# Kernel tuning notes

Hardware: AMD Instinct MI355X
Metric: run time of the kernel (lower is better)

Reference implementation:

```python
import jax, jax.numpy as jnp
import numpy as np

V, E, H, Z = 32000, 256, 512, 64
B, T = 32, 128
PAD = 0


def _n(k, shape, s=0.05):
    return jax.random.normal(k, shape, jnp.float32) * s


def setup_inputs() -> dict:
    key = jax.random.key(0)
    ks = jax.random.split(key, 32)
    inp = {
        "x": jax.random.randint(ks[0], (B, T), 0, V),
        "y": jax.random.randint(ks[1], (B, T), 0, V),
        "epsilon": jax.random.normal(ks[2], (Z,), jnp.float32),
        "enc_emb": _n(ks[3], (V, E)).at[PAD].set(0.0),  # padding_idx row zeroed
        "dec_emb": _n(ks[4], (V, E)),
        "fwd_Wih": _n(ks[5], (4 * H, E)), "fwd_Whh": _n(ks[6], (4 * H, H)), "fwd_b": _n(ks[7], (4 * H,)),
        "bwd_Wih": _n(ks[8], (4 * H, E)), "bwd_Whh": _n(ks[9], (4 * H, H)), "bwd_b": _n(ks[10], (4 * H,)),
        "dec_Wih": _n(ks[11], (4 * H, E)), "dec_Whh": _n(ks[12], (4 * H, H)), "dec_b": _n(ks[13], (4 * H,)),
        "enc_hW": _n(ks[14], (H, 2 * H)), "enc_hb": _n(ks[15], (H,)),
        "mu_W": _n(ks[16], (Z, H)), "mu_b": _n(ks[17], (Z,)),
        "std_W": _n(ks[18], (Z, H)), "std_b": _n(ks[19], (Z,)),
        "dec_hW": _n(ks[20], (H, Z)), "dec_hb": _n(ks[21], (H,)),
        "out_W": _n(ks[22], (V, H)), "out_b": _n(ks[23], (V,)),
    }
    return inp


def lstm_scan(e, h0, c0, Wih, Whh, b):
    # e: [B,T,E]; returns all hidden states [B,T,H] and final (h,c)
    def step(carry, x_t):
        h, c = carry
        g = x_t @ Wih.T + h @ Whh.T + b  # [B,4H], torch gate order i,f,g,o
        i, f, gg, o = jnp.split(g, 4, axis=-1)
        c = jax.nn.sigmoid(f) * c + jax.nn.sigmoid(i) * jnp.tanh(gg)
        h = jax.nn.sigmoid(o) * jnp.tanh(c)
        return (h, c), h
    (hT, cT), hs = jax.lax.scan(step, (h0, c0), jnp.swapaxes(e, 0, 1))
    return jnp.swapaxes(hs, 0, 1), hT, cT


def reference(x, y, epsilon, enc_emb, dec_emb,
              fwd_Wih, fwd_Whh, fwd_b, bwd_Wih, bwd_Whh, bwd_b,
              dec_Wih, dec_Whh, dec_b, enc_hW, enc_hb,
              mu_W, mu_b, std_W, std_b, dec_hW, dec_hb, out_W, out_b):
    Bx = x.shape[0]
    zeros = jnp.zeros((Bx, H), jnp.float32)
    # ---- encoder: two unidirectional LSTMs (second over flipped seq) ----
    ef = enc_emb[x]                 # [B,T,E]
    eb = enc_emb[x[:, ::-1]]
    _, hf, _ = lstm_scan(ef, zeros, zeros, fwd_Wih, fwd_Whh, fwd_b)
    _, hb, _ = lstm_scan(eb, zeros, zeros, bwd_Wih, bwd_Whh, bwd_b)
    h = jnp.concatenate([hf, hb], axis=1) @ enc_hW.T + enc_hb  # [B,H] (no activation)
    mu = h @ mu_W.T + mu_b
    sigma = jax.nn.softplus(h @ std_W.T + std_b)
    # ---- reparameterization (single epsilon shared across batch, as in torch) ----
    z = mu + sigma * epsilon        # [B,Z]
    # ---- decoder ----
    h0 = jnp.tanh(z @ dec_hW.T + dec_hb)  # [B,H]
    ed = dec_emb[x]
    hs, _, _ = lstm_scan(ed, h0, jnp.zeros_like(h0), dec_Wih, dec_Whh, dec_b)  # [B,T,H]
    logits = hs @ out_W.T + out_b   # [B,T,V]
    # ---- losses ----
    logp = jax.nn.log_softmax(logits.reshape(-1, V), axis=-1)
    ce = -jnp.take_along_axis(logp, y.reshape(-1, 1), axis=1).sum()
    kl = -0.5 * (1.0 + jnp.log(sigma) - mu ** 2 - sigma).sum()
    return (kl + ce) / Bx
```

## Files before the change

kernel.cpp:

```cpp
#include <hip/hip_runtime.h>
#include <hip/hip_bf16.h>

typedef float f32x4 __attribute__((ext_vector_type(4)));
typedef short s16x8 __attribute__((ext_vector_type(8)));
typedef unsigned int u32;
typedef unsigned short u16;

#define DEV static __device__ __forceinline__

namespace {
constexpr int V = 32000, E = 256, H = 512, Z = 64, B = 32, T = 128;
constexpr u32 POISON = 0xFFFFFFFFu;
constexpr int GUARD = 1 << 20;

constexpr size_t OFF_ZF   = 0;
constexpr size_t OFF_ZB   = 32768;
constexpr size_t OFF_PF   = 65536;
constexpr size_t OFF_PB   = OFF_PF + (size_t)T * 32768;
constexpr size_t OFF_H0   = OFF_PB + (size_t)T * 32768;
constexpr size_t OFF_HENC = OFF_H0 + 32768;
constexpr size_t OFF_HS   = OFF_HENC + 32768;
constexpr size_t OFF_LGY  = OFF_HS + (size_t)B*T*H*2;
constexpr size_t OFF_CER  = OFF_LGY + 16384;
constexpr size_t OFF_PEND = OFF_CER + 16384;
constexpr size_t OFF_Z    = OFF_PEND;
constexpr size_t OFF_KLP  = OFF_Z + 8192;
constexpr size_t OFF_WB   = OFF_KLP + 256;
constexpr size_t OFF_CEP  = OFF_PF;
}

DEV u16 f2b(float f) {
  u32 x = __builtin_bit_cast(u32, f);
  return (u16)((x + 0x7fffu + ((x >> 16) & 1u)) >> 16);
}
DEV float b2f(u16 u) {
  u32 x = ((u32)u) << 16;
  return __builtin_bit_cast(float, x);
}
DEV float fsig(float x) { return 1.f / (1.f + __expf(-x)); }
DEV float ftanh(float x) { return 2.f / (1.f + __expf(-2.f * x)) - 1.f; }

DEV u32 aload(const u32* p) { return __hip_atomic_load(p, __ATOMIC_RELAXED, __HIP_MEMORY_SCOPE_AGENT); }
DEV void astore(u32* p, u32 v) { __hip_atomic_store(p, v, __ATOMIC_RELAXED, __HIP_MEMORY_SCOPE_AGENT); }
DEV void afstore(u32* p, float v) { astore(p, __builtin_bit_cast(u32, v)); }

DEV u32* hslot(char* ws, int dir, int s) {
  size_t off = (s == 0) ? (dir ? OFF_ZB : OFF_ZF)
                        : ((dir ? OFF_PB : OFF_PF) + (size_t)(s - 1) * 32768);
  return reinterpret_cast<u32*>(ws + off);
}

__global__ __launch_bounds__(512, 1) void phaseA_k(
    const int* __restrict__ x, const float* __restrict__ emb,
    const float* __restrict__ fWih, const float* __restrict__ fWhh, const float* __restrict__ fb,
    const float* __restrict__ bWih, const float* __restrict__ bWhh, const float* __restrict__ bb,
    const float* __restrict__ enc_hW, const float* __restrict__ enc_hb,
    const float* __restrict__ mu_W, const float* __restrict__ mu_b,
    const float* __restrict__ std_W, const float* __restrict__ std_b,
    const float* __restrict__ epsv, const float* __restrict__ out_W,
    char* __restrict__ ws)
{
  __shared__ __align__(16) u16 Wl[64][776];
  __shared__ __align__(16) u16 act[32][776];
  __shared__ __align__(16) float gates[64][33];

  const int tid = threadIdx.x;
  const int wg = blockIdx.x;

  if (wg >= 64) {
    const size_t total = (size_t)V * H / 8;
    for (size_t idx = (size_t)(wg - 64) * 512 + tid; idx < total; idx += (size_t)128 * 512) {
      const float4* src = reinterpret_cast<const float4*>(out_W + idx * 8);
      float4 a = src[0], b = src[1];
      s16x8 o;
      o[0] = (short)f2b(a.x); o[1] = (short)f2b(a.y); o[2] = (short)f2b(a.z); o[3] = (short)f2b(a.w);
      o[4] = (short)f2b(b.x); o[5] = (short)f2b(b.y); o[6] = (short)f2b(b.z); o[7] = (short)f2b(b.w);
      *reinterpret_cast<s16x8*>(ws + OFF_WB + idx * 16) = o;
    }
    return;
  }

  const bool bwd = wg >= 32;
  const int dir = bwd ? 1 : 0;
  const int lw = wg & 31;
  const int u0 = lw * 16;
  const float* Wih = bwd ? bWih : fWih;
  const float* Whh = bwd ? bWhh : fWhh;
  const float* bv  = bwd ? bb : fb;

  {
    int r = tid >> 3, s8 = tid & 7;
    int grow = (r & 3) * H + u0 + (r >> 2);
    for (int kc = s8 * 96; kc < s8 * 96 + 96; kc += 8) {
      const float4* p;
      if (kc < E) p = reinterpret_cast<const float4*>(Wih + (size_t)grow * E + kc);
      else        p = reinterpret_cast<const float4*>(Whh + (size_t)grow * H + (kc - E));
      float4 a = p[0], b4 = p[1];
      Wl[r][kc+0] = f2b(a.x);  Wl[r][kc+1] = f2b(a.y);  Wl[r][kc+2] = f2b(a.z);  Wl[r][kc+3] = f2b(a.w);
      Wl[r][kc+4] = f2b(b4.x); Wl[r][kc+5] = f2b(b4.y); Wl[r][kc+6] = f2b(b4.z); Wl[r][kc+7] = f2b(b4.w);
    }
  }

  const int ab = tid >> 4, au = tid & 15;
  const int wv = tid >> 6, lane = tid & 63, l15 = lane & 15, lhi = lane >> 4;
  const int mq = wv & 3, nh = wv >> 2;
  const int unit = u0 + mq * 4 + lhi;
  const int batch = nh * 16 + l15;
  const float Bi = bv[0*H + unit], Bf = bv[1*H + unit];
  const float Bg = bv[2*H + unit], Bo = bv[3*H + unit];
  float c = 0.f;
  u32* actu = reinterpret_cast<u32*>(&act[0][0]);

  auto stage_emb = [&](int t) {
    int tt = bwd ? (T - 1 - t) : t;
    const float* src = emb + (size_t)x[ab * T + tt] * E + au * 16;
    const float4* s4 = reinterpret_cast<const float4*>(src);
    float4 A0 = s4[0], A1 = s4[1], A2 = s4[2], A3 = s4[3];
    u32 w0 = f2b(A0.x) | ((u32)f2b(A0.y) << 16);
    u32 w1 = f2b(A0.z) | ((u32)f2b(A0.w) << 16);
    u32 w2 = f2b(A1.x) | ((u32)f2b(A1.y) << 16);
    u32 w3 = f2b(A1.z) | ((u32)f2b(A1.w) << 16);
    u32 w4 = f2b(A2.x) | ((u32)f2b(A2.y) << 16);
    u32 w5 = f2b(A2.z) | ((u32)f2b(A2.w) << 16);
    u32 w6 = f2b(A3.x) | ((u32)f2b(A3.y) << 16);
    u32 w7 = f2b(A3.z) | ((u32)f2b(A3.w) << 16);
    u32* dst = actu + ab * 388 + au * 8;
    reinterpret_cast<uint4*>(dst)[0] = make_uint4(w0, w1, w2, w3);
    reinterpret_cast<uint4*>(dst)[1] = make_uint4(w4, w5, w6, w7);
  };

  stage_emb(0);

  for (int t = 0; t < T; ++t) {
    {
      const u32* hsrc = hslot(ws, dir, t);
      u32 tmp[16];
      #pragma unroll
      for (int j = 0; j < 16; ++j) tmp[j] = aload(hsrc + tid + j * 512);
      int guard = 0;
      while (true) {
        bool bad = false;
        #pragma unroll
        for (int j = 0; j < 16; ++j)
          if (tmp[j] == POISON) { bad = true; tmp[j] = aload(hsrc + tid + j * 512); }
        if (!bad || ++guard > GUARD) break;
        __builtin_amdgcn_s_sleep(1);
      }
      #pragma unroll
      for (int j = 0; j < 16; ++j) {
        int i = tid + j * 512;
        actu[(i >> 8) * 388 + 128 + (i & 255)] = tmp[j];
      }
    }
    __syncthreads();

    {
      f32x4 ac0 = {0,0,0,0}, ac1 = {0,0,0,0}, ac2 = {0,0,0,0}, ac3 = {0,0,0,0};
      #pragma unroll
      for (int s = 0; s < 6; ++s) {
        int kk = s * 128 + lhi * 8;
        s16x8 A0 = *reinterpret_cast<const s16x8*>(&Wl[mq * 16 + l15][kk]);
        s16x8 B0 = *reinterpret_cast<const s16x8*>(&act[nh * 16 + l15][kk]);
        ac0 = __builtin_amdgcn_mfma_f32_16x16x32_bf16(A0, B0, ac0, 0, 0, 0);
        s16x8 A1 = *reinterpret_cast<const s16x8*>(&Wl[mq * 16 + l15][kk + 32]);
        s16x8 B1 = *reinterpret_cast<const s16x8*>(&act[nh * 16 + l15][kk + 32]);
        ac1 = __builtin_amdgcn_mfma_f32_16x16x32_bf16(A1, B1, ac1, 0, 0, 0);
        s16x8 A2 = *reinterpret_cast<const s16x8*>(&Wl[mq * 16 + l15][kk + 64]);
        s16x8 B2 = *reinterpret_cast<const s16x8*>(&act[nh * 16 + l15][kk + 64]);
        ac2 = __builtin_amdgcn_mfma_f32_16x16x32_bf16(A2, B2, ac2, 0, 0, 0);
        s16x8 A3 = *reinterpret_cast<const s16x8*>(&Wl[mq * 16 + l15][kk + 96]);
        s16x8 B3 = *reinterpret_cast<const s16x8*>(&act[nh * 16 + l15][kk + 96]);
        ac3 = __builtin_amdgcn_mfma_f32_16x16x32_bf16(A3, B3, ac3, 0, 0, 0);
      }
      f32x4 ac = (ac0 + ac1) + (ac2 + ac3);
      float gi = ac[0] + Bi, gf = ac[1] + Bf, gg = ac[2] + Bg, go = ac[3] + Bo;
      c = fsig(gf) * c + fsig(gi) * ftanh(gg);
      float h = fsig(go) * ftanh(c);
      u32 bits = f2b(h);
      u32 other = (u32)__shfl_down((int)bits, 16);
      if ((lhi & 1) == 0) {
        u32* dst = hslot(ws, dir, t + 1) + batch * 256 + (unit >> 1);
        astore(dst, bits | (other << 16));
      }
    }
    __syncthreads();
    if (t != T - 1) stage_emb(t + 1);
  }

  {
    u32* wlu = reinterpret_cast<u32*>(&Wl[0][0]);
    const u32* hf = hslot(ws, 0, T);
    const u32* hb = hslot(ws, 1, T);
    u32 tmp[32];
    #pragma unroll
    for (int j = 0; j < 32; ++j) {
      int i = tid + j * 512, b = i >> 9, k = i & 511;
      tmp[j] = (k < 256) ? aload(hf + b * 256 + k) : aload(hb + b * 256 + (k - 256));
    }
    int guard = 0;
    while (true) {
      bool bad = false;
      #pragma unroll
      for (int j = 0; j < 32; ++j)
        if (tmp[j] == POISON) {
          bad = true;
          int i = tid + j * 512, b = i >> 9, k = i & 511;
          tmp[j] = (k < 256) ? aload(hf + b * 256 + k) : aload(hb + b * 256 + (k - 256));
        }
      if (!bad || ++guard > GUARD) break;
      __builtin_amdgcn_s_sleep(1);
    }
    #pragma unroll
    for (int j = 0; j < 32; ++j) wlu[tid + j * 512] = tmp[j];
  }
  __syncthreads();
  if (tid < 256) {
    const u16* hcat = &Wl[0][0];
    int b = tid >> 3, jc = tid & 7;
    int j = wg * 8 + jc;
    float s = enc_hb[j];
    const float4* w4 = reinterpret_cast<const float4*>(enc_hW + (size_t)j * 1024);
    for (int kk = 0; kk < 256; ++kk) {
      float4 wv4 = w4[kk];
      const u16* hp = hcat + b * 1024 + kk * 4;
      s += wv4.x * b2f(hp[0]) + wv4.y * b2f(hp[1]) + wv4.z * b2f(hp[2]) + wv4.w * b2f(hp[3]);
    }
    u32 bits = f2b(s);
    u32 other = (u32)__shfl_down((int)bits, 1);
    if ((jc & 1) == 0) {
      u32* dst = reinterpret_cast<u32*>(ws + OFF_HENC) + b * 256 + j / 2;
      astore(dst, bits | (other << 16));
    }
  }
  __syncthreads();

  {
    u32* hhu = reinterpret_cast<u32*>(&act[0][0]);
    const u32* he = reinterpret_cast<const u32*>(ws + OFF_HENC);
    u32 tmp[16];
    #pragma unroll
    for (int j = 0; j < 16; ++j) tmp[j] = aload(he + tid + j * 512);
    int guard = 0;
    while (true) {
      bool bad = false;
      #pragma unroll
      for (int j = 0; j < 16; ++j)
        if (tmp[j] == POISON) { bad = true; tmp[j] = aload(he + tid + j * 512); }
      if (!bad || ++guard > GUARD) break;
      __builtin_amdgcn_s_sleep(1);
    }
    #pragma unroll
    for (int j = 0; j < 16; ++j) hhu[tid + j * 512] = tmp[j];
  }
  __syncthreads();
  {
    const u16* hh = &act[0][0];
    int b = tid >> 4, l16 = tid & 15;
    float pm = 0.f, ps = 0.f;
    const float* mwr = mu_W + (size_t)wg * H;
    const float* swr = std_W + (size_t)wg * H;
    for (int k = l16 * 32; k < l16 * 32 + 32; ++k) {
      float hv = b2f(hh[b * H + k]);
      pm += mwr[k] * hv;
      ps += swr[k] * hv;
    }
    gates[b][l16] = pm;
    gates[32 + b][l16] = ps;
  }
  __syncthreads();
  if (tid < 32) {
    int b = tid;
    float mu = mu_b[wg], sv = std_b[wg];
    for (int l = 0; l < 16; ++l) { mu += gates[b][l]; sv += gates[32 + b][l]; }
    float sig = fmaxf(sv, 0.f) + log1pf(__expf(-fabsf(sv)));
    float zv = mu + sig * epsv[wg];
    reinterpret_cast<float*>(ws + OFF_Z)[b * Z + wg] = zv;
    gates[b][16] = -0.5f * (1.f + logf(sig) - mu * mu - sig);
  }
  __syncthreads();
  if (tid == 0) {
    float kl = 0.f;
    for (int b = 0; b < 32; ++b) kl += gates[b][16];
    reinterpret_cast<float*>(ws + OFF_KLP)[wg] = kl;
  }
}

__global__ __launch_bounds__(512, 1) void phaseB_k(
    const int* __restrict__ x, const int* __restrict__ y,
    const float* __restrict__ emb,
    const float* __restrict__ Wih, const float* __restrict__ Whh, const float* __restrict__ bv,
    const float* __restrict__ dec_hW, const float* __restrict__ dec_hb,
    const float* __restrict__ out_W, const float* __restrict__ out_b,
    char* __restrict__ ws, float* __restrict__ out)
{
  __shared__ __align__(16) char smem[157440];
  const int tid = threadIdx.x;
  const int bid = blockIdx.x;
  u32* hsu = reinterpret_cast<u32*>(ws + OFF_HS);
  const int wid = tid >> 6, lane = tid & 63, l15 = lane & 15, lhi = lane >> 4;

  if (bid < 32) {
    u16 (*Wl)[776]  = reinterpret_cast<u16(*)[776]>(smem);
    u16 (*act)[776] = reinterpret_cast<u16(*)[776]>(smem + 99328);
    const int wg = bid;
    const int u0 = wg * 16;

    {
      int r = tid >> 3, s8 = tid & 7;
      int grow = (r & 3) * H + u0 + (r >> 2);
      for (int kc = s8 * 96; kc < s8 * 96 + 96; kc += 8) {
        const float4* p;
        if (kc < E) p = reinterpret_cast<const float4*>(Wih + (size_t)grow * E + kc);
        else        p = reinterpret_cast<const float4*>(Whh + (size_t)grow * H + (kc - E));
        float4 a = p[0], b4 = p[1];
        Wl[r][kc+0] = f2b(a.x);  Wl[r][kc+1] = f2b(a.y);  Wl[r][kc+2] = f2b(a.z);  Wl[r][kc+3] = f2b(a.w);
        Wl[r][kc+4] = f2b(b4.x); Wl[r][kc+5] = f2b(b4.y); Wl[r][kc+6] = f2b(b4.z); Wl[r][kc+7] = f2b(b4.w);
      }
    }

    const int ab = tid >> 4, au = tid & 15;
    const int mq = wid & 3, nh = wid >> 2;
    const int unit = u0 + mq * 4 + lhi;
    const int batch = nh * 16 + l15;
    const float Bi = bv[0*H + unit], Bf = bv[1*H + unit];
    const float Bg = bv[2*H + unit], Bo = bv[3*H + unit];
    float c = 0.f;

    u32* h0u = reinterpret_cast<u32*>(ws + OFF_H0);
    const float* zws = reinterpret_cast<const float*>(ws + OFF_Z);
    u32* actu = reinterpret_cast<u32*>(&act[0][0]);

    auto stage_emb = [&](int t) {
      const float* src = emb + (size_t)x[ab * T + t] * E + au * 16;
      const float4* s4 = reinterpret_cast<const float4*>(src);
      float4 A0 = s4[0], A1 = s4[1], A2 = s4[2], A3 = s4[3];
      u32 w0 = f2b(A0.x) | ((u32)f2b(A0.y) << 16);
      u32 w1 = f2b(A0.z) | ((u32)f2b(A0.w) << 16);
      u32 w2 = f2b(A1.x) | ((u32)f2b(A1.y) << 16);
      u32 w3 = f2b(A1.z) | ((u32)f2b(A1.w) << 16);
      u32 w4 = f2b(A2.x) | ((u32)f2b(A2.y) << 16);
      u32 w5 = f2b(A2.z) | ((u32)f2b(A2.w) << 16);
      u32 w6 = f2b(A3.x) | ((u32)f2b(A3.y) << 16);
      u32 w7 = f2b(A3.z) | ((u32)f2b(A3.w) << 16);
      u32* dst = actu + ab * 388 + au * 8;
      reinterpret_cast<uint4*>(dst)[0] = make_uint4(w0, w1, w2, w3);
      reinterpret_cast<uint4*>(dst)[1] = make_uint4(w4, w5, w6, w7);
    };

    stage_emb(0);

    {
      float s = dec_hb[u0 + au];
      const float* wr = dec_hW + (size_t)(u0 + au) * Z;
      for (int zz = 0; zz < Z; ++zz) s += wr[zz] * zws[ab * Z + zz];
      float h0 = ftanh(s);
      u32 bits = f2b(h0);
      u32 other = (u32)__shfl_down((int)bits, 1);
      if ((au & 1) == 0) astore(h0u + ab * 256 + (u0 + au) / 2, bits | (other << 16));
    }

    for (int t = 0; t < T; ++t) {
      {
        u32 tmp[16];
        const u32* base = (t == 0) ? h0u : (hsu + (size_t)(t - 1) * B * 256);
        #pragma unroll
        for (int j = 0; j < 16; ++j) tmp[j] = aload(base + tid + j * 512);
        int guard = 0;
        while (true) {
          bool bad = false;
          #pragma unroll
          for (int j = 0; j < 16; ++j)
            if (tmp[j] == POISON) { bad = true; tmp[j] = aload(base + tid + j * 512); }
          if (!bad || ++guard > GUARD) break;
          __builtin_amdgcn_s_sleep(1);
        }
        #pragma unroll
        for (int j = 0; j < 16; ++j) {
          int i = tid + j * 512;
          actu[(i >> 8) * 388 + 128 + (i & 255)] = tmp[j];
        }
      }
      __syncthreads();

      {
        f32x4 ac0 = {0,0,0,0}, ac1 = {0,0,0,0}, ac2 = {0,0,0,0}, ac3 = {0,0,0,0};
        #pragma unroll
        for (int s = 0; s < 6; ++s) {
          int kk = s * 128 + lhi * 8;
          s16x8 A0 = *reinterpret_cast<const s16x8*>(&Wl[mq * 16 + l15][kk]);
          s16x8 B0 = *reinterpret_cast<const s16x8*>(&act[nh * 16 + l15][kk]);
          ac0 = __builtin_amdgcn_mfma_f32_16x16x32_bf16(A0, B0, ac0, 0, 0, 0);
          s16x8 A1 = *reinterpret_cast<const s16x8*>(&Wl[mq * 16 + l15][kk + 32]);
          s16x8 B1 = *reinterpret_cast<const s16x8*>(&act[nh * 16 + l15][kk + 32]);
          ac1 = __builtin_amdgcn_mfma_f32_16x16x32_bf16(A1, B1, ac1, 0, 0, 0);
          s16x8 A2 = *reinterpret_cast<const s16x8*>(&Wl[mq * 16 + l15][kk + 64]);
          s16x8 B2 = *reinterpret_cast<const s16x8*>(&act[nh * 16 + l15][kk + 64]);
          ac2 = __builtin_amdgcn_mfma_f32_16x16x32_bf16(A2, B2, ac2, 0, 0, 0);
          s16x8 A3 = *reinterpret_cast<const s16x8*>(&Wl[mq * 16 + l15][kk + 96]);
          s16x8 B3 = *reinterpret_cast<const s16x8*>(&act[nh * 16 + l15][kk + 96]);
          ac3 = __builtin_amdgcn_mfma_f32_16x16x32_bf16(A3, B3, ac3, 0, 0, 0);
        }
        f32x4 ac = (ac0 + ac1) + (ac2 + ac3);
        float gi = ac[0] + Bi, gf = ac[1] + Bf, gg = ac[2] + Bg, go = ac[3] + Bo;
        c = fsig(gf) * c + fsig(gi) * ftanh(gg);
        float h = fsig(go) * ftanh(c);
        u32 bits = f2b(h);
        u32 other = (u32)__shfl_down((int)bits, 16);
        if ((lhi & 1) == 0) {
          u32* dst = hsu + (size_t)(t * B + batch) * 256 + (unit >> 1);
          astore(dst, bits | (other << 16));
        }
      }
      __syncthreads();
      if (t != T - 1) stage_emb(t + 1);
    }
    return;
  }

  const int w = bid - 32;
  u16 (*At)[72] = reinterpret_cast<u16(*)[72]>(smem);
  u16 (*Bt)[72] = reinterpret_cast<u16(*)[72]>(smem + 18432);
  float* red = reinterpret_cast<float*>(smem + 55296);
  const u16* Wb = reinterpret_cast<const u16*>(ws + OFF_WB);
  const int wm = wid & 1, wn = wid >> 1;
  const int sr = tid >> 3, ss = tid & 7;

  for (int tl = w; tl < 4000; tl += 192) {
    const int rt = tl / 125, ct = tl % 125;
    const int row0 = rt * 128, col0 = ct * 256;

    f32x4 acc[4][4];
    #pragma unroll
    for (int i = 0; i < 4; ++i)
      #pragma unroll
      for (int j = 0; j < 4; ++j) acc[i][j] = {0, 0, 0, 0};

    for (int kt = 0; kt < 8; ++kt) {
      #pragma unroll
      for (int it = 0; it < 2; ++it) {
        int r = it * 64 + sr;
        const u32* p = hsu + (size_t)(row0 + r) * 256 + kt * 32 + ss * 4;
        u32 a0 = aload(p), a1 = aload(p + 1), a2 = aload(p + 2), a3 = aload(p + 3);
        int guard = 0;
        while ((a0 == POISON || a1 == POISON || a2 == POISON || a3 == POISON) && ++guard <= GUARD) {
          __builtin_amdgcn_s_sleep(64);
          a0 = aload(p); a1 = aload(p + 1); a2 = aload(p + 2); a3 = aload(p + 3);
        }
        u32* d = reinterpret_cast<u32*>(&At[r][ss * 8]);
        d[0] = a0; d[1] = a1; d[2] = a2; d[3] = a3;
      }
      #pragma unroll
      for (int it = 0; it < 4; ++it) {
        int r = it * 64 + sr;
        *reinterpret_cast<s16x8*>(&Bt[r][ss * 8]) =
            *reinterpret_cast<const s16x8*>(Wb + (size_t)(col0 + r) * H + kt * 64 + ss * 8);
      }
      __syncthreads();
      #pragma unroll
      for (int ks = 0; ks < 2; ++ks) {
        int kk = ks * 32 + lhi * 8;
        s16x8 af[4], bf[4];
        #pragma unroll
        for (int mi = 0; mi < 4; ++mi)
          af[mi] = *reinterpret_cast<const s16x8*>(&At[wm * 64 + mi * 16 + l15][kk]);
        #pragma unroll
        for (int ni = 0; ni < 4; ++ni)
          bf[ni] = *reinterpret_cast<const s16x8*>(&Bt[wn * 64 + ni * 16 + l15][kk]);
        #pragma unroll
        for (int mi = 0; mi < 4; ++mi)
          #pragma unroll
          for (int ni = 0; ni < 4; ++ni)
            acc[mi][ni] = __builtin_amdgcn_mfma_f32_16x16x32_bf16(af[mi], bf[ni], acc[mi][ni], 0, 0, 0);
      }
      __syncthreads();
    }

    float bias[4];
    #pragma unroll
    for (int ni = 0; ni < 4; ++ni) bias[ni] = out_b[col0 + wn * 64 + ni * 16 + l15];

    #pragma unroll
    for (int mi = 0; mi < 4; ++mi) {
      #pragma unroll
      for (int reg = 0; reg < 4; ++reg) {
        float l0 = acc[mi][0][reg] + bias[0];
        float l1 = acc[mi][1][reg] + bias[1];
        float l2 = acc[mi][2][reg] + bias[2];
        float l3 = acc[mi][3][reg] + bias[3];
        float m = fmaxf(fmaxf(l0, l1), fmaxf(l2, l3));
        for (int d = 1; d < 16; d <<= 1) m = fmaxf(m, __shfl_xor(m, d, 16));
        float s = __expf(l0 - m) + __expf(l1 - m) + __expf(l2 - m) + __expf(l3 - m);
        for (int d = 1; d < 16; d <<= 1) s += __shfl_xor(s, d, 16);
        if (l15 == 0) {
          int lr = mi * 16 + lhi * 4 + reg;
          red[((wm * 64 + lr) * 4 + wn) * 2 + 0] = m;
          red[((wm * 64 + lr) * 4 + wn) * 2 + 1] = s;
        }
      }
    }
    __syncthreads();
    if (tid < 128) {
      int lr = tid;
      float M = -3.0e38f, S = 0.f;
      #pragma unroll
      for (int wnn = 0; wnn < 4; ++wnn) {
        float m = red[(lr * 4 + wnn) * 2 + 0];
        float s = red[(lr * 4 + wnn) * 2 + 1];
        float nm = fmaxf(M, m);
        S = S * __expf(M - nm) + s * __expf(m - nm);
        M = nm;
      }
      u32* cepw = reinterpret_cast<u32*>(ws + OFF_CEP);
      size_t ix = ((size_t)(row0 + lr) * 125 + ct) * 2;
      afstore(cepw + ix + 0, M);
      afstore(cepw + ix + 1, S);
    }
    __syncthreads();
  }

  for (int r = w * 8 + wid; r < 4096; r += 192 * 8) {
    int t = r >> 5, b = r & 31;
    int yy = y[b * T + t];
    const u32* hp = hsu + (size_t)r * 256 + lane * 4;
    u32 a0 = aload(hp), a1 = aload(hp + 1), a2 = aload(hp + 2), a3 = aload(hp + 3);
    int guard = 0;
    while ((a0 == POISON || a1 == POISON || a2 == POISON || a3 == POISON) && ++guard <= GUARD) {
      __builtin_amdgcn_s_sleep(64);
      a0 = aload(hp); a1 = aload(hp + 1); a2 = aload(hp + 2); a3 = aload(hp + 3);
    }
    const float4* wp = reinterpret_cast<const float4*>(out_W + (size_t)yy * H + lane * 8);
    float4 w0 = wp[0], w1 = wp[1];
    float s = b2f((u16)(a0 & 0xFFFF)) * w0.x + b2f((u16)(a0 >> 16)) * w0.y
            + b2f((u16)(a1 & 0xFFFF)) * w0.z + b2f((u16)(a1 >> 16)) * w0.w
            + b2f((u16)(a2 & 0xFFFF)) * w1.x + b2f((u16)(a2 >> 16)) * w1.y
            + b2f((u16)(a3 & 0xFFFF)) * w1.z + b2f((u16)(a3 >> 16)) * w1.w;
    for (int d = 1; d < 64; d <<= 1) s += __shfl_xor(s, d);
    if (lane == 0)
      afstore(reinterpret_cast<u32*>(ws + OFF_LGY) + r, s + out_b[yy]);
  }

  {
    int r = w * 512 + tid;
    if (r < 4096) {
      const u32* lgyu = reinterpret_cast<const u32*>(ws + OFF_LGY);
      u32 lb = aload(lgyu + r);
      int guard = 0;
      while (lb == POISON && ++guard <= GUARD) { __builtin_amdgcn_s_sleep(64); lb = aload(lgyu + r); }
      float ly = __builtin_bit_cast(float, lb);
      const u32* cp = reinterpret_cast<const u32*>(ws + OFF_CEP);
      float M = -3.0e38f, S = 0.f;
      for (int cch = 0; cch < 125; ++cch) {
        size_t ix = ((size_t)r * 125 + cch) * 2;
        u32 ma = aload(cp + ix), sa = aload(cp + ix + 1);
        int g2 = 0;
        while ((ma == POISON || sa == POISON) && ++g2 <= GUARD) {
          __builtin_amdgcn_s_sleep(64);
          ma = aload(cp + ix); sa = aload(cp + ix + 1);
        }
        float m = __builtin_bit_cast(float, ma), s = __builtin_bit_cast(float, sa);
        float nm = fmaxf(M, m);
        S = S * __expf(M - nm) + s * __expf(m - nm);
        M = nm;
      }
      afstore(reinterpret_cast<u32*>(ws + OFF_CER) + r, M + logf(S) - ly);
    }
  }

  if (w == 0) {
    __syncthreads();
    float* rb = reinterpret_cast<float*>(smem);
    const u32* ceru = reinterpret_cast<const u32*>(ws + OFF_CER);
    const float* klp = reinterpret_cast<const float*>(ws + OFF_KLP);
    float s = 0.f;
    for (int j = 0; j < 8; ++j) {
      int r = tid + j * 512;
      u32 v = aload(ceru + r);
      int guard = 0;
      while (v == POISON && ++guard <= GUARD) { __builtin_amdgcn_s_sleep(64); v = aload(ceru + r); }
      s += __builtin_bit_cast(float, v);
    }
    if (tid < 64) s += klp[tid];
    rb[tid] = s;
    __syncthreads();
    for (int d = 256; d > 0; d >>= 1) {
      if (tid < d) rb[tid] += rb[tid + d];
      __syncthreads();
    }
    if (tid == 0) out[0] = rb[0] / 32.f;
  }
}

extern "C" void kernel_launch(void* const* d_in, const int* in_sizes, int n_in,
                              void* d_out, int out_size, void* d_ws, size_t ws_size,
                              hipStream_t stream) {
  (void)in_sizes; (void)n_in; (void)out_size; (void)ws_size;
  const int*   x       = (const int*)d_in[0];
  const int*   y       = (const int*)d_in[1];
  const float* epsv    = (const float*)d_in[2];
  const float* enc_emb = (const float*)d_in[3];
  const float* dec_emb = (const float*)d_in[4];
  const float* fWih    = (const float*)d_in[5];
  const float* fWhh    = (const float*)d_in[6];
  const float* fb      = (const float*)d_in[7];
  const float* bWih    = (const float*)d_in[8];
  const float* bWhh    = (const float*)d_in[9];
  const float* bb      = (const float*)d_in[10];
  const float* dWih    = (const float*)d_in[11];
  const float* dWhh    = (const float*)d_in[12];
  const float* db      = (const float*)d_in[13];
  const float* enc_hW  = (const float*)d_in[14];
  const float* enc_hb  = (const float*)d_in[15];
  const float* mu_W    = (const float*)d_in[16];
  const float* mu_b    = (const float*)d_in[17];
  const float* std_W   = (const float*)d_in[18];
  const float* std_b   = (const float*)d_in[19];
  const float* dec_hW  = (const float*)d_in[20];
  const float* dec_hb  = (const float*)d_in[21];
  const float* out_W   = (const float*)d_in[22];
  const float* out_b   = (const float*)d_in[23];
  char* ws = (char*)d_ws;

  hipMemsetAsync(ws + OFF_ZF, 0x00, 65536, stream);
  hipMemsetAsync(ws + OFF_PF, 0xFF, OFF_PEND - OFF_PF, stream);

  phaseA_k<<<192, 512, 0, stream>>>(x, enc_emb, fWih, fWhh, fb, bWih, bWhh, bb,
                                    enc_hW, enc_hb, mu_W, mu_b, std_W, std_b,
                                    epsv, out_W, ws);

  hipMemsetAsync(ws + OFF_CEP, 0xFF, 4096000, stream);

  phaseB_k<<<224, 512, 0, stream>>>(x, y, dec_emb, dWih, dWhh, db, dec_hW, dec_hb,
                                    out_W, out_b, ws, (float*)d_out);
}
```

Measured before the change: 1.165 ms.

## Load recurrent hidden state directly into MFMA registers, transpose CE partial layout

In the encoder and decoder LSTM recurrences, each lane now polls and loads the exact previous hidden-state fragments it needs for its MFMA B operand straight from global memory into registers. This replaces cooperatively staging the whole h vector into shared memory and removes the barrier that staging required before the matmul. The shared activation buffer shrinks to hold only the embedding part. Separately, the cross-entropy partial (max, sum) array is stored column-chunk-major so the final reduction reads it coalesced across threads. In exchange, each lane issues more redundant global loads and holds 64 extra registers, and an extra barrier is added after staging the embedding.

```diff
diff --git a/kernel.cpp b/kernel.cpp
--- a/kernel.cpp
+++ b/kernel.cpp
@@ -5,6 +5,7 @@
 typedef short s16x8 __attribute__((ext_vector_type(8)));
 typedef unsigned int u32;
 typedef unsigned short u16;
+typedef u32 u32x4v __attribute__((ext_vector_type(4)));
 
 #define DEV static __device__ __forceinline__
 
@@ -50,6 +51,20 @@
   return reinterpret_cast<u32*>(ws + off);
 }
 
+DEV void pollload_h(const u32* hb_, int lhi, u32 (&hv)[64]) {
+  #pragma unroll
+  for (int i = 0; i < 64; ++i) hv[i] = aload(hb_ + (i >> 2) * 16 + lhi * 4 + (i & 3));
+  int guard = 0;
+  while (true) {
+    bool bad = false;
+    #pragma unroll
+    for (int i = 0; i < 64; ++i)
+      if (hv[i] == POISON) { bad = true; hv[i] = aload(hb_ + (i >> 2) * 16 + lhi * 4 + (i & 3)); }
+    if (!bad || ++guard > GUARD) break;
+    __builtin_amdgcn_s_sleep(1);
+  }
+}
+
 __global__ __launch_bounds__(512, 1) void phaseA_k(
     const int* __restrict__ x, const float* __restrict__ emb,
     const float* __restrict__ fWih, const float* __restrict__ fWhh, const float* __restrict__ fb,
@@ -61,7 +76,7 @@
     char* __restrict__ ws)
 {
   __shared__ __align__(16) u16 Wl[64][776];
-  __shared__ __align__(16) u16 act[32][776];
+  __shared__ __align__(16) u16 actE[32][256];
   __shared__ __align__(16) float gates[64][33];
 
   const int tid = threadIdx.x;
@@ -109,7 +124,7 @@
   const float Bi = bv[0*H + unit], Bf = bv[1*H + unit];
   const float Bg = bv[2*H + unit], Bo = bv[3*H + unit];
   float c = 0.f;
-  u32* actu = reinterpret_cast<u32*>(&act[0][0]);
+  u32* actu = reinterpret_cast<u32*>(&actE[0][0]);
 
   auto stage_emb = [&](int t) {
     int tt = bwd ? (T - 1 - t) : t;
@@ -124,56 +139,42 @@
     u32 w5 = f2b(A2.z) | ((u32)f2b(A2.w) << 16);
     u32 w6 = f2b(A3.x) | ((u32)f2b(A3.y) << 16);
     u32 w7 = f2b(A3.z) | ((u32)f2b(A3.w) << 16);
-    u32* dst = actu + ab * 388 + au * 8;
+    u32* dst = actu + ab * 128 + au * 8;
     reinterpret_cast<uint4*>(dst)[0] = make_uint4(w0, w1, w2, w3);
     reinterpret_cast<uint4*>(dst)[1] = make_uint4(w4, w5, w6, w7);
   };
 
   stage_emb(0);
+  __syncthreads();
+
+  const u16* wrow = &Wl[mq * 16 + l15][0];
+  const u16* arow = &actE[nh * 16 + l15][0];
 
   for (int t = 0; t < T; ++t) {
+    u32 hv[64];
+    pollload_h(hslot(ws, dir, t) + batch * 256, lhi, hv);
+
     {
-      const u32* hsrc = hslot(ws, dir, t);
-      u32 tmp[16];
-      #pragma unroll
-      for (int j = 0; j < 16; ++j) tmp[j] = aload(hsrc + tid + j * 512);
-      int guard = 0;
-      while (true) {
-        bool bad = false;
-        #pragma unroll
-        for (int j = 0; j < 16; ++j)
-          if (tmp[j] == POISON) { bad = true; tmp[j] = aload(hsrc + tid + j * 512); }
-        if (!bad || ++guard > GUARD) break;
-        __builtin_amdgcn_s_sleep(1);
-      }
-      #pragma unroll
-      for (int j = 0; j < 16; ++j) {
-        int i = tid + j * 512;
-        actu[(i >> 8) * 388 + 128 + (i & 255)] = tmp[j];
-      }
-    }
-    __syncthreads();
-
-    {
-      f32x4 ac0 = {0,0,0,0}, ac1 = {0,0,0,0}, ac2 = {0,0,0,0}, ac3 = {0,0,0,0};
-      #pragma unroll
-      for (int s = 0; s < 6; ++s) {
-        int kk = s * 128 + lhi * 8;
-        s16x8 A0 = *reinterpret_cast<const s16x8*>(&Wl[mq * 16 + l15][kk]);
-        s16x8 B0 = *reinterpret_cast<const s16x8*>(&act[nh * 16 + l15][kk]);
-        ac0 = __builtin_amdgcn_mfma_f32_16x16x32_bf16(A0, B0, ac0, 0, 0, 0);
-        s16x8 A1 = *reinterpret_cast<const s16x8*>(&Wl[mq * 16 + l15][kk + 32]);
-        s16x8 B1 = *reinterpret_cast<const s16x8*>(&act[nh * 16 + l15][kk + 32]);
-        ac1 = __builtin_amdgcn_mfma_f32_16x16x32_bf16(A1, B1, ac1, 0, 0, 0);
-        s16x8 A2 = *reinterpret_cast<const s16x8*>(&Wl[mq * 16 + l15][kk + 64]);
-        s16x8 B2 = *reinterpret_cast<const s16x8*>(&act[nh * 16 + l15][kk + 64]);
-        ac2 = __builtin_amdgcn_mfma_f32_16x16x32_bf16(A2, B2, ac2, 0, 0, 0);
-        s16x8 A3 = *reinterpret_cast<const s16x8*>(&Wl[mq * 16 + l15][kk + 96]);
-        s16x8 B3 = *reinterpret_cast<const s16x8*>(&act[nh * 16 + l15][kk + 96]);
-        ac3 = __builtin_amdgcn_mfma_f32_16x16x32_bf16(A3, B3, ac3, 0, 0, 0);
-      }
-      f32x4 ac = (ac0 + ac1) + (ac2 + ac3);
-      float gi = ac[0] + Bi, gf = ac[1] + Bf, gg = ac[2] + Bg, go = ac[3] + Bo;
+      f32x4 ac[4];
+      #pragma unroll
+      for (int i = 0; i < 4; ++i) ac[i] = {0, 0, 0, 0};
+      #pragma unroll
+      for (int fe = 0; fe < 8; ++fe) {
+        int kk = fe * 32 + lhi * 8;
+        s16x8 A = *reinterpret_cast<const s16x8*>(wrow + kk);
+        s16x8 Bv = *reinterpret_cast<const s16x8*>(arow + kk);
+        ac[fe & 3] = __builtin_amdgcn_mfma_f32_16x16x32_bf16(A, Bv, ac[fe & 3], 0, 0, 0);
+      }
+      #pragma unroll
+      for (int f = 0; f < 16; ++f) {
+        int kk = 256 + f * 32 + lhi * 8;
+        s16x8 A = *reinterpret_cast<const s16x8*>(wrow + kk);
+        u32x4v bw = {hv[4*f], hv[4*f+1], hv[4*f+2], hv[4*f+3]};
+        s16x8 Bv = __builtin_bit_cast(s16x8, bw);
+        ac[f & 3] = __builtin_amdgcn_mfma_f32_16x16x32_bf16(A, Bv, ac[f & 3], 0, 0, 0);
+      }
+      f32x4 acs = (ac[0] + ac[1]) + (ac[2] + ac[3]);
+      float gi = acs[0] + Bi, gf = acs[1] + Bf, gg = acs[2] + Bg, go = acs[3] + Bo;
       c = fsig(gf) * c + fsig(gi) * ftanh(gg);
       float h = fsig(go) * ftanh(c);
       u32 bits = f2b(h);
@@ -184,7 +185,7 @@
       }
     }
     __syncthreads();
-    if (t != T - 1) stage_emb(t + 1);
+    if (t != T - 1) { stage_emb(t + 1); __syncthreads(); }
   }
 
   {
@@ -235,7 +236,7 @@
   __syncthreads();
 
   {
-    u32* hhu = reinterpret_cast<u32*>(&act[0][0]);
+    u32* hhu = reinterpret_cast<u32*>(&Wl[0][0]);
     const u32* he = reinterpret_cast<const u32*>(ws + OFF_HENC);
     u32 tmp[16];
     #pragma unroll
@@ -249,12 +250,13 @@
       if (!bad || ++guard > GUARD) break;
       __builtin_amdgcn_s_sleep(1);
     }
+    __syncthreads();
     #pragma unroll
     for (int j = 0; j < 16; ++j) hhu[tid + j * 512] = tmp[j];
   }
   __syncthreads();
   {
-    const u16* hh = &act[0][0];
+    const u16* hh = &Wl[0][0];
     int b = tid >> 4, l16 = tid & 15;
     float pm = 0.f, ps = 0.f;
     const float* mwr = mu_W + (size_t)wg * H;
@@ -300,8 +302,8 @@
   const int wid = tid >> 6, lane = tid & 63, l15 = lane & 15, lhi = lane >> 4;
 
   if (bid < 32) {
-    u16 (*Wl)[776]  = reinterpret_cast<u16(*)[776]>(smem);
-    u16 (*act)[776] = reinterpret_cast<u16(*)[776]>(smem + 99328);
+    u16 (*Wl)[776]   = reinterpret_cast<u16(*)[776]>(smem);
+    u16 (*actE)[256] = reinterpret_cast<u16(*)[256]>(smem + 99328);
     const int wg = bid;
     const int u0 = wg * 16;
 
@@ -328,7 +330,7 @@
 
     u32* h0u = reinterpret_cast<u32*>(ws + OFF_H0);
     const float* zws = reinterpret_cast<const float*>(ws + OFF_Z);
-    u32* actu = reinterpret_cast<u32*>(&act[0][0]);
+    u32* actu = reinterpret_cast<u32*>(&actE[0][0]);
 
     auto stage_emb = [&](int t) {
       const float* src = emb + (size_t)x[ab * T + t] * E + au * 16;
@@ -342,7 +344,7 @@
       u32 w5 = f2b(A2.z) | ((u32)f2b(A2.w) << 16);
       u32 w6 = f2b(A3.x) | ((u32)f2b(A3.y) << 16);
       u32 w7 = f2b(A3.z) | ((u32)f2b(A3.w) << 16);
-      u32* dst = actu + ab * 388 + au * 8;
+      u32* dst = actu + ab * 128 + au * 8;
       reinterpret_cast<uint4*>(dst)[0] = make_uint4(w0, w1, w2, w3);
       reinterpret_cast<uint4*>(dst)[1] = make_uint4(w4, w5, w6, w7);
     };
@@ -358,50 +360,37 @@
       u32 other = (u32)__shfl_down((int)bits, 1);
       if ((au & 1) == 0) astore(h0u + ab * 256 + (u0 + au) / 2, bits | (other << 16));
     }
+    __syncthreads();
+
+    const u16* wrow = &Wl[mq * 16 + l15][0];
+    const u16* arow = &actE[nh * 16 + l15][0];
 
     for (int t = 0; t < T; ++t) {
+      const u32* base = (t == 0) ? h0u : (hsu + (size_t)(t - 1) * B * 256);
+      u32 hv[64];
+      pollload_h(base + batch * 256, lhi, hv);
+
       {
-        u32 tmp[16];
-        const u32* base = (t == 0) ? h0u : (hsu + (size_t)(t - 1) * B * 256);
+        f32x4 ac[4];
         #pragma unroll
-        for (int j = 0; j < 16; ++j) tmp[j] = aload(base + tid + j * 512);
-        int guard = 0;
-        while (true) {
-          bool bad = false;
-          #pragma unroll
-          for (int j = 0; j < 16; ++j)
-            if (tmp[j] == POISON) { bad = true; tmp[j] = aload(base + tid + j * 512); }
-          if (!bad || ++guard > GUARD) break;
-          __builtin_amdgcn_s_sleep(1);
+        for (int i = 0; i < 4; ++i) ac[i] = {0, 0, 0, 0};
+        #pragma unroll
+        for (int fe = 0; fe < 8; ++fe) {
+          int kk = fe * 32 + lhi * 8;
+          s16x8 A = *reinterpret_cast<const s16x8*>(wrow + kk);
+          s16x8 Bv = *reinterpret_cast<const s16x8*>(arow + kk);
+          ac[fe & 3] = __builtin_amdgcn_mfma_f32_16x16x32_bf16(A, Bv, ac[fe & 3], 0, 0, 0);
         }
         #pragma unroll
-        for (int j = 0; j < 16; ++j) {
-          int i = tid + j * 512;
-          actu[(i >> 8) * 388 + 128 + (i & 255)] = tmp[j];
+        for (int f = 0; f < 16; ++f) {
+          int kk = 256 + f * 32 + lhi * 8;
+          s16x8 A = *reinterpret_cast<const s16x8*>(wrow + kk);
+          u32x4v bw = {hv[4*f], hv[4*f+1], hv[4*f+2], hv[4*f+3]};
+          s16x8 Bv = __builtin_bit_cast(s16x8, bw);
+          ac[f & 3] = __builtin_amdgcn_mfma_f32_16x16x32_bf16(A, Bv, ac[f & 3], 0, 0, 0);
         }
-      }
-      __syncthreads();
-
-      {
-        f32x4 ac0 = {0,0,0,0}, ac1 = {0,0,0,0}, ac2 = {0,0,0,0}, ac3 = {0,0,0,0};
-        #pragma unroll
-        for (int s = 0; s < 6; ++s) {
-          int kk = s * 128 + lhi * 8;
-          s16x8 A0 = *reinterpret_cast<const s16x8*>(&Wl[mq * 16 + l15][kk]);
-          s16x8 B0 = *reinterpret_cast<const s16x8*>(&act[nh * 16 + l15][kk]);
-          ac0 = __builtin_amdgcn_mfma_f32_16x16x32_bf16(A0, B0, ac0, 0, 0, 0);
-          s16x8 A1 = *reinterpret_cast<const s16x8*>(&Wl[mq * 16 + l15][kk + 32]);
-          s16x8 B1 = *reinterpret_cast<const s16x8*>(&act[nh * 16 + l15][kk + 32]);
-          ac1 = __builtin_amdgcn_mfma_f32_16x16x32_bf16(A1, B1, ac1, 0, 0, 0);
-          s16x8 A2 = *reinterpret_cast<const s16x8*>(&Wl[mq * 16 + l15][kk + 64]);
-          s16x8 B2 = *reinterpret_cast<const s16x8*>(&act[nh * 16 + l15][kk + 64]);
-          ac2 = __builtin_amdgcn_mfma_f32_16x16x32_bf16(A2, B2, ac2, 0, 0, 0);
-          s16x8 A3 = *reinterpret_cast<const s16x8*>(&Wl[mq * 16 + l15][kk + 96]);
-          s16x8 B3 = *reinterpret_cast<const s16x8*>(&act[nh * 16 + l15][kk + 96]);
-          ac3 = __builtin_amdgcn_mfma_f32_16x16x32_bf16(A3, B3, ac3, 0, 0, 0);
-        }
-        f32x4 ac = (ac0 + ac1) + (ac2 + ac3);
-        float gi = ac[0] + Bi, gf = ac[1] + Bf, gg = ac[2] + Bg, go = ac[3] + Bo;
+        f32x4 acs = (ac[0] + ac[1]) + (ac[2] + ac[3]);
+        float gi = acs[0] + Bi, gf = acs[1] + Bf, gg = acs[2] + Bg, go = acs[3] + Bo;
         c = fsig(gf) * c + fsig(gi) * ftanh(gg);
         float h = fsig(go) * ftanh(c);
         u32 bits = f2b(h);
@@ -412,7 +401,7 @@
         }
       }
       __syncthreads();
-      if (t != T - 1) stage_emb(t + 1);
+      if (t != T - 1) { stage_emb(t + 1); __syncthreads(); }
     }
     return;
   }
@@ -511,7 +500,7 @@
         M = nm;
       }
       u32* cepw = reinterpret_cast<u32*>(ws + OFF_CEP);
-      size_t ix = ((size_t)(row0 + lr) * 125 + ct) * 2;
+      size_t ix = ((size_t)ct * 4096 + row0 + lr) * 2;
       afstore(cepw + ix + 0, M);
       afstore(cepw + ix + 1, S);
     }
@@ -550,7 +539,7 @@
       const u32* cp = reinterpret_cast<const u32*>(ws + OFF_CEP);
       float M = -3.0e38f, S = 0.f;
       for (int cch = 0; cch < 125; ++cch) {
-        size_t ix = ((size_t)r * 125 + cch) * 2;
+        size_t ix = ((size_t)cch * 4096 + r) * 2;
         u32 ma = aload(cp + ix), sa = aload(cp + ix + 1);
         int g2 = 0;
         while ((ma == POISON || sa == POISON) && ++g2 <= GUARD) {
```

Measured after the change: 4.441 ms. +281.1%, slower.
